# Optimization experiments

Measured on AMD Instinct MI355X. Metric: run time of the kernel, lower is better.

Reference implementation:

```python
import jax, jax.numpy as jnp
import numpy as np

B, T, E, H = 2, 2048, 768, 12
DH = E // H  # per-head attention dim
EPS = 1e-5


def setup_inputs() -> dict:
    key = jax.random.key(0)
    ks = jax.random.split(key, 12)
    s = 0.02
    return {
        "x": jax.random.normal(ks[0], (B, T, E), dtype=jnp.float32),
        # stacked per-head projection weights: [H, E, DH], biases [H, DH]
        "Wq": jax.random.normal(ks[1], (H, E, DH), dtype=jnp.float32) * s,
        "bq": jax.random.normal(ks[2], (H, DH), dtype=jnp.float32) * s,
        "Wk": jax.random.normal(ks[3], (H, E, DH), dtype=jnp.float32) * s,
        "bk": jax.random.normal(ks[4], (H, DH), dtype=jnp.float32) * s,
        "Wv": jax.random.normal(ks[5], (H, E, DH), dtype=jnp.float32) * s,
        "bv": jax.random.normal(ks[6], (H, DH), dtype=jnp.float32) * s,
        "Wo": jax.random.normal(ks[7], (E, E), dtype=jnp.float32) * s,
        "bo": jax.random.normal(ks[8], (E,), dtype=jnp.float32) * s,
        "gamma": jnp.ones((E,), dtype=jnp.float32),
        "beta": jnp.zeros((E,), dtype=jnp.float32),
    }


def reference(x, Wq, bq, Wk, bk, Wv, bv, Wo, bo, gamma, beta):
    # per-head projections (heads stacked on axis h)
    q = jnp.einsum("bte,hed->bhtd", x, Wq) + bq[None, :, None, :]
    k = jnp.einsum("bte,hed->bhtd", x, Wk) + bk[None, :, None, :]
    v = jnp.einsum("bte,hed->bhtd", x, Wv) + bv[None, :, None, :]

    scores = jnp.einsum("bhtd,bhsd->bhts", q, k) / jnp.sqrt(jnp.float32(DH))
    causal = jnp.tril(jnp.ones((T, T), dtype=bool))  # True = keep
    scores = jnp.where(causal[None, None], scores, -jnp.inf)
    attn = jax.nn.softmax(scores, axis=-1)
    o = jnp.einsum("bhts,bhsd->bhtd", attn, v)  # [B,H,T,DH]

    # concat heads in head order -> [B,T,E]
    concat = jnp.transpose(o, (0, 2, 1, 3)).reshape(B, T, E)
    proj = concat @ Wo + bo

    # LayerNorm(proj) then residual add
    mu = jnp.mean(proj, axis=-1, keepdims=True)
    var = jnp.mean((proj - mu) ** 2, axis=-1, keepdims=True)
    normed = (proj - mu) * jax.lax.rsqrt(var + EPS) * gamma + beta
    return x + normed
```

## Files before the change

### kernel.cpp

```cpp
#include <hip/hip_runtime.h>
#include <stdint.h>

#define NROWS 4096
#define EMB   768
#define NQKV  2304
#define TSEQ  2048
#define NHEAD 12
#define NBH   24

typedef unsigned short u16;
typedef u16  ushort8 __attribute__((ext_vector_type(8)));
typedef __bf16 bf16x8 __attribute__((ext_vector_type(8)));
typedef float f32x4 __attribute__((ext_vector_type(4)));

typedef const __attribute__((address_space(1))) void* gas_ptr;
typedef __attribute__((address_space(3))) void* las_ptr;

__device__ __forceinline__ u16 f2bf(float f) {
  union { float f; uint32_t u; } v; v.f = f;
  uint32_t u = v.u;
  return (u16)((u + 0x7fffu + ((u >> 16) & 1u)) >> 16);
}
__device__ __forceinline__ uint32_t cvtpk(float lo, float hi) {
  uint32_t r;
  asm("v_cvt_pk_bf16_f32 %0, %1, %2" : "=v"(r) : "v"(lo), "v"(hi));
  return r;
}

#define VMCNT2 asm volatile("s_waitcnt vmcnt(2)" ::: "memory")
#define VMCNT0 asm volatile("s_waitcnt vmcnt(0)" ::: "memory")
#define LGKM0  asm volatile("s_waitcnt lgkmcnt(0)" ::: "memory")
#define SBAR   __builtin_amdgcn_s_barrier()
#define SCHED0 __builtin_amdgcn_sched_barrier(0)

__global__ __launch_bounds__(256) void k_pack_x(const float* __restrict__ x, u16* __restrict__ xb) {
  int i = (blockIdx.x * 256 + threadIdx.x) * 8;
  float4 a = *(const float4*)(x + i);
  float4 b = *(const float4*)(x + i + 4);
  uint4 o;
  o.x = cvtpk(a.x, a.y); o.y = cvtpk(a.z, a.w);
  o.z = cvtpk(b.x, b.y); o.w = cvtpk(b.z, b.w);
  *(uint4*)(xb + i) = o;
}

__global__ __launch_bounds__(256) void k_pack_wqkv(const float* __restrict__ Wq, const float* __restrict__ Wk,
                            const float* __restrict__ Wv, const float* __restrict__ bq,
                            const float* __restrict__ bk, const float* __restrict__ bv,
                            u16* __restrict__ wt, float* __restrict__ bias) {
  int idx = blockIdx.x * 256 + threadIdx.x;
  if (idx >= NQKV * EMB) return;
  int n = idx / EMB, e = idx - n * EMB;
  int sel = n / EMB;
  int c = n - sel * EMB;
  int h = c >> 6, d = c & 63;
  const float* W = sel == 0 ? Wq : (sel == 1 ? Wk : Wv);
  wt[idx] = f2bf(W[((size_t)h * EMB + e) * 64 + d]);
  if (e == 0) {
    const float* bs = sel == 0 ? bq : (sel == 1 ? bk : bv);
    bias[n] = bs[h * 64 + d];
  }
}

__global__ __launch_bounds__(256) void k_pack_wo(const float* __restrict__ Wo, u16* __restrict__ wot) {
  int idx = blockIdx.x * 256 + threadIdx.x;
  if (idx >= EMB * EMB) return;
  int n = idx / EMB, e = idx - n * EMB;
  wot[idx] = f2bf(Wo[(size_t)e * EMB + n]);
}

template<int OUT_F32>
__global__ __launch_bounds__(256) void k_gemm(const u16* __restrict__ A, const u16* __restrict__ Bt,
                                              const float* __restrict__ bias, void* __restrict__ Cout,
                                              int M, int N, int K) {
  __shared__ u16 lds_a[128 * 32];
  __shared__ u16 lds_b[128 * 32];
  int tid = threadIdx.x;
  int w = tid >> 6, lane = tid & 63;
  int wr = w >> 1, wc = w & 1;
  int m0 = blockIdx.x * 128, n0 = blockIdx.y * 128;
  int lrow = lane & 15, lk8 = (lane >> 4) * 8;

  f32x4 zero = {0.f, 0.f, 0.f, 0.f};
  f32x4 acc[4][4];
  for (int m = 0; m < 4; ++m) for (int n = 0; n < 4; ++n) acc[m][n] = zero;

  int sr = tid >> 2;
  int sk = (tid & 3) * 8;

  for (int k0 = 0; k0 < K; k0 += 32) {
#pragma unroll
    for (int c = 0; c < 2; ++c) {
      int r = c * 64 + sr;
      const u16* ga = A  + (size_t)(m0 + r) * K + k0 + sk;
      const u16* gb = Bt + (size_t)(n0 + r) * K + k0 + sk;
      u16* la = lds_a + c * 2048 + w * 512;
      u16* lb = lds_b + c * 2048 + w * 512;
      __builtin_amdgcn_global_load_lds((gas_ptr)ga, (las_ptr)la, 16, 0, 0);
      __builtin_amdgcn_global_load_lds((gas_ptr)gb, (las_ptr)lb, 16, 0, 0);
    }
    __syncthreads();
    bf16x8 af[4], bfr[4];
#pragma unroll
    for (int m = 0; m < 4; ++m)
      af[m] = *(const bf16x8*)(lds_a + (wr * 64 + m * 16 + lrow) * 32 + lk8);
#pragma unroll
    for (int n = 0; n < 4; ++n)
      bfr[n] = *(const bf16x8*)(lds_b + (wc * 64 + n * 16 + lrow) * 32 + lk8);
#pragma unroll
    for (int m = 0; m < 4; ++m)
#pragma unroll
      for (int n = 0; n < 4; ++n)
        acc[m][n] = __builtin_amdgcn_mfma_f32_16x16x32_bf16(af[m], bfr[n], acc[m][n], 0, 0, 0);
    __syncthreads();
  }

#pragma unroll
  for (int m = 0; m < 4; ++m)
#pragma unroll
    for (int n = 0; n < 4; ++n) {
      int col = n0 + wc * 64 + n * 16 + lrow;
      float bcol = bias[col];
#pragma unroll
      for (int r = 0; r < 4; ++r) {
        int row = m0 + wr * 64 + m * 16 + (lane >> 4) * 4 + r;
        float v = acc[m][n][r] + bcol;
        if (OUT_F32) ((float*)Cout)[(size_t)row * N + col] = v;
        else         ((u16*)Cout)[(size_t)row * N + col] = f2bf(v);
      }
    }
}

__global__ __launch_bounds__(256) void k_transpose_v(const u16* __restrict__ qkv, u16* __restrict__ vt) {
  __shared__ u16 lds[64][65];
  int bh = blockIdx.y;
  int b = bh / NHEAD, h = bh - b * NHEAD;
  int t0 = blockIdx.x * 64;
  int tid = threadIdx.x;
  int r = tid >> 2, c0 = (tid & 3) * 16;
  const u16* src = qkv + (size_t)(b * TSEQ + t0 + r) * NQKV + 2 * EMB + h * 64 + c0;
  ushort8 v0 = *(const ushort8*)(src);
  ushort8 v1 = *(const ushort8*)(src + 8);
#pragma unroll
  for (int j = 0; j < 8; ++j) { lds[r][c0 + j] = v0[j]; lds[r][c0 + 8 + j] = v1[j]; }
  __syncthreads();
  int d = tid >> 2, tt = (tid & 3) * 16;
  ushort8 o0, o1;
#pragma unroll
  for (int j = 0; j < 8; ++j) { o0[j] = lds[tt + j][d]; o1[j] = lds[tt + 8 + j][d]; }
  u16* dst = vt + (size_t)(bh * 64 + d) * TSEQ + t0 + tt;
  *(ushort8*)dst = o0;
  *(ushort8*)(dst + 8) = o1;
}

__global__ __launch_bounds__(256) void k_attn(const u16* __restrict__ qkv, const u16* __restrict__ vt,
                                              u16* __restrict__ aout) {
  __shared__ u16 kbuf[3][64 * 64];
  __shared__ u16 vbuf[2][64 * 64];
  __shared__ u16 pbuf[4][16 * 64];
  int tid = threadIdx.x;
  int w = tid >> 6, lane = tid & 63;
  int ql = lane & 15, g = lane >> 4;
  int bid = blockIdx.x;
  int xcd = bid & 7, slot = bid >> 3;
  int y = xcd * 3 + (slot >> 5);
  int qblk = 31 - (slot & 31);
  int b = y / NHEAD, h = y - b * NHEAD;
  int nt = qblk + 1;
  int qrow0w = qblk * 64 + w * 16;
  int qg = qrow0w + ql;

  const u16* qp = qkv + (size_t)(b * TSEQ + qg) * NQKV + h * 64;
  bf16x8 bq0 = *(const bf16x8*)(qp + g * 8);
  bf16x8 bq1 = *(const bf16x8*)(qp + 32 + g * 8);

  const u16* kst = qkv + (size_t)(b * TSEQ) * NQKV + EMB + h * 64;
  const u16* vst = vt + (size_t)y * 64 * TSEQ;
  int srow = tid >> 3, scol = tid & 7;

  f32x4 zero = {0.f, 0.f, 0.f, 0.f};
  f32x4 o[4]; for (int n = 0; n < 4; ++n) o[n] = zero;
  float lr = 0.f;
  const float sc2 = 0.18033688f;
  u16* pw = &pbuf[w][0];
  int swz = (ql & 7) << 3;

  auto STAGE_K = [&](int bi, int t_) {
#pragma unroll
    for (int i = 0; i < 2; ++i) {
      int row = i * 32 + srow;
      int c16 = scol ^ (row & 7);
      const u16* gk = kst + (size_t)(t_ * 64 + row) * NQKV + c16 * 8;
      __builtin_amdgcn_global_load_lds((gas_ptr)gk, (las_ptr)(&kbuf[bi][i * 2048 + w * 512]), 16, 0, 0);
    }
  };
  auto STAGE_V = [&](int bi, int t_) {
#pragma unroll
    for (int i = 0; i < 2; ++i) {
      int row = i * 32 + srow;
      int c16 = scol ^ (row & 7);
      const u16* gv = vst + (size_t)row * TSEQ + t_ * 64 + c16 * 8;
      __builtin_amdgcn_global_load_lds((gas_ptr)gv, (las_ptr)(&vbuf[bi][i * 2048 + w * 512]), 16, 0, 0);
    }
  };

  STAGE_V(0, 0);
  STAGE_K(0, 0);
  if (nt > 1) STAGE_K(1, 1);

  for (int t = 0; t < nt; ++t) {
    if (t + 1 < nt) VMCNT2; else VMCNT0;
    SBAR;
    if (t + 1 < nt) STAGE_V((t + 1) & 1, t + 1);
    if (t + 2 < nt) STAGE_K((t + 2) % 3, t + 2);

    const u16* kb = &kbuf[t % 3][0];
    const u16* vb = &vbuf[t & 1][0];
    int s0 = t * 64;

    f32x4 st[4];
#pragma unroll
    for (int sblk = 0; sblk < 4; ++sblk) {
      int row = sblk * 16 + ql;
      bf16x8 ka0 = *(const bf16x8*)(kb + ((row * 64 + 8 * g) ^ swz));
      bf16x8 ka1 = *(const bf16x8*)(kb + ((row * 64 + 32 + 8 * g) ^ swz));
      f32x4 acc = zero;
      acc = __builtin_amdgcn_mfma_f32_16x16x32_bf16(ka0, bq0, acc, 0, 0, 0);
      acc = __builtin_amdgcn_mfma_f32_16x16x32_bf16(ka1, bq1, acc, 0, 0, 0);
      st[sblk] = acc;
    }

    bool lastt = (t == nt - 1);
    float e[4][4];
#pragma unroll
    for (int sblk = 0; sblk < 4; ++sblk)
#pragma unroll
      for (int r = 0; r < 4; ++r) {
        float vv = __builtin_fmaf(st[sblk][r], sc2, -2.0f);
        if (lastt) {
          int sg = s0 + sblk * 16 + 4 * g + r;
          if (sg > qg) vv = -1e30f;
        }
        float ee = __builtin_amdgcn_exp2f(vv);
        e[sblk][r] = ee;
        lr += ee;
      }

#pragma unroll
    for (int sblk = 0; sblk < 4; ++sblk) {
      uint2 dw;
      dw.x = cvtpk(e[sblk][0], e[sblk][1]);
      dw.y = cvtpk(e[sblk][2], e[sblk][3]);
      *(uint2*)(pw + ((ql * 64 + sblk * 16 + 4 * g) ^ swz)) = dw;
    }
    LGKM0; SCHED0;
    bf16x8 ap0 = *(const bf16x8*)(pw + ((ql * 64 + 8 * g) ^ swz));
    bf16x8 ap1 = *(const bf16x8*)(pw + ((ql * 64 + 32 + 8 * g) ^ swz));

#pragma unroll
    for (int n = 0; n < 4; ++n) {
      int row = n * 16 + ql;
      bf16x8 vb0 = *(const bf16x8*)(vb + ((row * 64 + 8 * g) ^ swz));
      bf16x8 vb1 = *(const bf16x8*)(vb + ((row * 64 + 32 + 8 * g) ^ swz));
      o[n] = __builtin_amdgcn_mfma_f32_16x16x32_bf16(ap0, vb0, o[n], 0, 0, 0);
      o[n] = __builtin_amdgcn_mfma_f32_16x16x32_bf16(ap1, vb1, o[n], 0, 0, 0);
    }
  }

  lr += __shfl_xor(lr, 16);
  lr += __shfl_xor(lr, 32);
  float linv = 1.0f / lr;
  float li[4];
#pragma unroll
  for (int r = 0; r < 4; ++r) li[r] = __shfl(linv, 4 * g + r);
#pragma unroll
  for (int n = 0; n < 4; ++n)
#pragma unroll
    for (int r = 0; r < 4; ++r) {
      int q = qrow0w + 4 * g + r;
      aout[(size_t)(b * TSEQ + q) * EMB + h * 64 + n * 16 + ql] = f2bf(o[n][r] * li[r]);
    }
}

__global__ __launch_bounds__(256) void k_ln_res(const float* __restrict__ proj, const float* __restrict__ x,
                                                const float* __restrict__ gamma, const float* __restrict__ beta,
                                                float* __restrict__ out) {
  __shared__ float smem[2][4];
  int row = blockIdx.x;
  const float* pr = proj + (size_t)row * EMB;
  const float* xr = x + (size_t)row * EMB;
  float* orow = out + (size_t)row * EMB;
  int tid = threadIdx.x;
  float v[3];
  float s = 0.f, s2 = 0.f;
#pragma unroll
  for (int i = 0; i < 3; ++i) { v[i] = pr[tid + 256 * i]; s += v[i]; s2 += v[i] * v[i]; }
#pragma unroll
  for (int m = 1; m < 64; m <<= 1) { s += __shfl_xor(s, m); s2 += __shfl_xor(s2, m); }
  int w = tid >> 6, lane = tid & 63;
  if (lane == 0) { smem[0][w] = s; smem[1][w] = s2; }
  __syncthreads();
  s  = smem[0][0] + smem[0][1] + smem[0][2] + smem[0][3];
  s2 = smem[1][0] + smem[1][1] + smem[1][2] + smem[1][3];
  float mu = s * (1.f / EMB);
  float var = s2 * (1.f / EMB) - mu * mu;
  float rstd = rsqrtf(var + 1e-5f);
#pragma unroll
  for (int i = 0; i < 3; ++i) {
    int c = tid + 256 * i;
    orow[c] = xr[c] + (v[i] - mu) * rstd * gamma[c] + beta[c];
  }
}

extern "C" void kernel_launch(void* const* d_in, const int* in_sizes, int n_in,
                              void* d_out, int out_size, void* d_ws, size_t ws_size,
                              hipStream_t stream) {
  const float* x     = (const float*)d_in[0];
  const float* Wq    = (const float*)d_in[1];
  const float* bq    = (const float*)d_in[2];
  const float* Wk    = (const float*)d_in[3];
  const float* bk    = (const float*)d_in[4];
  const float* Wv    = (const float*)d_in[5];
  const float* bv    = (const float*)d_in[6];
  const float* Wo    = (const float*)d_in[7];
  const float* bo    = (const float*)d_in[8];
  const float* gamma = (const float*)d_in[9];
  const float* beta  = (const float*)d_in[10];
  float* out = (float*)d_out;

  char* ws = (char*)d_ws;
  size_t off = 0;
  u16* xb    = (u16*)(ws + off); off += (size_t)NROWS * EMB * 2;
  u16* wqkvt = (u16*)(ws + off); off += (size_t)NQKV * EMB * 2;
  u16* wot   = (u16*)(ws + off); off += (size_t)EMB * EMB * 2;
  float* bqkv = (float*)(ws + off); off += (size_t)NQKV * 4;
  u16* qkv   = (u16*)(ws + off); off += (size_t)NROWS * NQKV * 2;
  u16* vt    = (u16*)(ws + off); off += (size_t)NBH * 64 * TSEQ * 2;
  u16* aout  = (u16*)(ws + off); off += (size_t)NROWS * EMB * 2;
  float* proj = (float*)qkv;

  k_pack_x<<<NROWS * EMB / (256 * 8), 256, 0, stream>>>(x, xb);
  k_pack_wqkv<<<(NQKV * EMB + 255) / 256, 256, 0, stream>>>(Wq, Wk, Wv, bq, bk, bv, wqkvt, bqkv);
  k_pack_wo<<<(EMB * EMB + 255) / 256, 256, 0, stream>>>(Wo, wot);
  k_gemm<0><<<dim3(NROWS / 128, NQKV / 128), 256, 0, stream>>>(xb, wqkvt, bqkv, qkv, NROWS, NQKV, EMB);
  k_transpose_v<<<dim3(TSEQ / 64, NBH), 256, 0, stream>>>(qkv, vt);
  k_attn<<<dim3(768), 256, 0, stream>>>(qkv, vt, aout);
  k_gemm<1><<<dim3(NROWS / 128, EMB / 128), 256, 0, stream>>>(aout, wot, bo, proj, NROWS, EMB, EMB);
  k_ln_res<<<NROWS, 256, 0, stream>>>(proj, x, gamma, beta, out);
}
```

Baseline: 137.8 us.

## Fuse V transpose into QKV GEMM, persistent attention scheduler, swizzled K=64 GEMM tiles

The QKV GEMM epilogue now writes V directly in transposed layout, which removes the separate transpose kernel. The GEMM moves to a K-step of 64 with XOR-swizzled LDS tiles and is templated on tile shape, so the output projection can use 128x64 tiles for more blocks. Attention becomes a persistent kernel that pulls work from per-XCD atomic counters, giving dynamic load balance across the causal triangle. Its K/V staging is simplified to a double buffer with a full vmcnt(0) wait, which may expose more load latency than the previous triple-buffered K.

```diff
diff --git a/kernel.cpp b/kernel.cpp
--- a/kernel.cpp
+++ b/kernel.cpp
@@ -9,6 +9,7 @@
 #define NBH   24
 
 typedef unsigned short u16;
+typedef u16  ushort4v __attribute__((ext_vector_type(4)));
 typedef u16  ushort8 __attribute__((ext_vector_type(8)));
 typedef __bf16 bf16x8 __attribute__((ext_vector_type(8)));
 typedef float f32x4 __attribute__((ext_vector_type(4)));
@@ -27,11 +28,14 @@
   return r;
 }
 
-#define VMCNT2 asm volatile("s_waitcnt vmcnt(2)" ::: "memory")
 #define VMCNT0 asm volatile("s_waitcnt vmcnt(0)" ::: "memory")
 #define LGKM0  asm volatile("s_waitcnt lgkmcnt(0)" ::: "memory")
 #define SBAR   __builtin_amdgcn_s_barrier()
 #define SCHED0 __builtin_amdgcn_sched_barrier(0)
+
+__global__ void k_zero(uint32_t* cnt) {
+  if (threadIdx.x < 8) cnt[threadIdx.x] = 0;
+}
 
 __global__ __launch_bounds__(256) void k_pack_x(const float* __restrict__ x, u16* __restrict__ xb) {
   int i = (blockIdx.x * 256 + threadIdx.x) * 8;
@@ -68,217 +72,225 @@
   wot[idx] = f2bf(Wo[(size_t)e * EMB + n]);
 }
 
-template<int OUT_F32>
+template<int BM, int BN, int OUT_MODE>
 __global__ __launch_bounds__(256) void k_gemm(const u16* __restrict__ A, const u16* __restrict__ Bt,
                                               const float* __restrict__ bias, void* __restrict__ Cout,
-                                              int M, int N, int K) {
-  __shared__ u16 lds_a[128 * 32];
-  __shared__ u16 lds_b[128 * 32];
+                                              u16* __restrict__ vtout, int M, int N, int K) {
+  constexpr int MR = BM / 32, NR = BN / 32;
+  __shared__ u16 lds_a[BM * 64];
+  __shared__ u16 lds_b[BN * 64];
   int tid = threadIdx.x;
   int w = tid >> 6, lane = tid & 63;
   int wr = w >> 1, wc = w & 1;
-  int m0 = blockIdx.x * 128, n0 = blockIdx.y * 128;
-  int lrow = lane & 15, lk8 = (lane >> 4) * 8;
+  int m0 = blockIdx.x * BM, n0 = blockIdx.y * BN;
+  int lrow = lane & 15, g = lane >> 4;
 
   f32x4 zero = {0.f, 0.f, 0.f, 0.f};
-  f32x4 acc[4][4];
-  for (int m = 0; m < 4; ++m) for (int n = 0; n < 4; ++n) acc[m][n] = zero;
-
-  int sr = tid >> 2;
-  int sk = (tid & 3) * 8;
-
-  for (int k0 = 0; k0 < K; k0 += 32) {
-#pragma unroll
-    for (int c = 0; c < 2; ++c) {
-      int r = c * 64 + sr;
-      const u16* ga = A  + (size_t)(m0 + r) * K + k0 + sk;
-      const u16* gb = Bt + (size_t)(n0 + r) * K + k0 + sk;
-      u16* la = lds_a + c * 2048 + w * 512;
-      u16* lb = lds_b + c * 2048 + w * 512;
-      __builtin_amdgcn_global_load_lds((gas_ptr)ga, (las_ptr)la, 16, 0, 0);
-      __builtin_amdgcn_global_load_lds((gas_ptr)gb, (las_ptr)lb, 16, 0, 0);
+  f32x4 acc[MR][NR];
+  for (int m = 0; m < MR; ++m) for (int n = 0; n < NR; ++n) acc[m][n] = zero;
+
+  int l8 = lane >> 3, c8 = lane & 7;
+
+  for (int k0 = 0; k0 < K; k0 += 64) {
+#pragma unroll
+    for (int i = 0; i < BM / 32; ++i) {
+      int row = w * (BM / 4) + 8 * i + l8;
+      int c16 = c8 ^ (row & 7);
+      const u16* ga = A + (size_t)(m0 + row) * K + k0 + c16 * 8;
+      __builtin_amdgcn_global_load_lds((gas_ptr)ga, (las_ptr)(lds_a + (w * (BM / 4) + 8 * i) * 64), 16, 0, 0);
+    }
+#pragma unroll
+    for (int i = 0; i < BN / 32; ++i) {
+      int row = w * (BN / 4) + 8 * i + l8;
+      int c16 = c8 ^ (row & 7);
+      const u16* gb = Bt + (size_t)(n0 + row) * K + k0 + c16 * 8;
+      __builtin_amdgcn_global_load_lds((gas_ptr)gb, (las_ptr)(lds_b + (w * (BN / 4) + 8 * i) * 64), 16, 0, 0);
     }
     __syncthreads();
-    bf16x8 af[4], bfr[4];
-#pragma unroll
-    for (int m = 0; m < 4; ++m)
-      af[m] = *(const bf16x8*)(lds_a + (wr * 64 + m * 16 + lrow) * 32 + lk8);
-#pragma unroll
-    for (int n = 0; n < 4; ++n)
-      bfr[n] = *(const bf16x8*)(lds_b + (wc * 64 + n * 16 + lrow) * 32 + lk8);
-#pragma unroll
-    for (int m = 0; m < 4; ++m)
-#pragma unroll
-      for (int n = 0; n < 4; ++n)
-        acc[m][n] = __builtin_amdgcn_mfma_f32_16x16x32_bf16(af[m], bfr[n], acc[m][n], 0, 0, 0);
+    bf16x8 af[MR][2], bfr[NR][2];
+#pragma unroll
+    for (int m = 0; m < MR; ++m)
+#pragma unroll
+      for (int kc = 0; kc < 2; ++kc) {
+        int row = wr * (BM / 2) + m * 16 + lrow;
+        int ch = (kc * 4 + g) ^ (row & 7);
+        af[m][kc] = *(const bf16x8*)(lds_a + row * 64 + ch * 8);
+      }
+#pragma unroll
+    for (int n = 0; n < NR; ++n)
+#pragma unroll
+      for (int kc = 0; kc < 2; ++kc) {
+        int row = wc * (BN / 2) + n * 16 + lrow;
+        int ch = (kc * 4 + g) ^ (row & 7);
+        bfr[n][kc] = *(const bf16x8*)(lds_b + row * 64 + ch * 8);
+      }
+#pragma unroll
+    for (int kc = 0; kc < 2; ++kc)
+#pragma unroll
+      for (int m = 0; m < MR; ++m)
+#pragma unroll
+        for (int n = 0; n < NR; ++n)
+          acc[m][n] = __builtin_amdgcn_mfma_f32_16x16x32_bf16(af[m][kc], bfr[n][kc], acc[m][n], 0, 0, 0);
     __syncthreads();
   }
 
 #pragma unroll
-  for (int m = 0; m < 4; ++m)
-#pragma unroll
-    for (int n = 0; n < 4; ++n) {
-      int col = n0 + wc * 64 + n * 16 + lrow;
+  for (int m = 0; m < MR; ++m)
+#pragma unroll
+    for (int n = 0; n < NR; ++n) {
+      int col = n0 + wc * (BN / 2) + n * 16 + lrow;
       float bcol = bias[col];
-#pragma unroll
-      for (int r = 0; r < 4; ++r) {
-        int row = m0 + wr * 64 + m * 16 + (lane >> 4) * 4 + r;
-        float v = acc[m][n][r] + bcol;
-        if (OUT_F32) ((float*)Cout)[(size_t)row * N + col] = v;
-        else         ((u16*)Cout)[(size_t)row * N + col] = f2bf(v);
+      int row0 = m0 + wr * (BM / 2) + m * 16 + 4 * g;
+      if (OUT_MODE == 2 && col >= 2 * EMB) {
+        int c = col - 2 * EMB;
+        int hh = c >> 6, d = c & 63;
+        int bb = row0 >> 11, t = row0 & 2047;
+        int y = bb * NHEAD + hh;
+        ushort4v pk;
+#pragma unroll
+        for (int r = 0; r < 4; ++r) pk[r] = f2bf(acc[m][n][r] + bcol);
+        *(ushort4v*)(vtout + (size_t)(y * 64 + d) * TSEQ + t) = pk;
+      } else {
+#pragma unroll
+        for (int r = 0; r < 4; ++r) {
+          int row = row0 + r;
+          float v = acc[m][n][r] + bcol;
+          if (OUT_MODE == 1) ((float*)Cout)[(size_t)row * N + col] = v;
+          else               ((u16*)Cout)[(size_t)row * N + col] = f2bf(v);
+        }
       }
     }
 }
 
-__global__ __launch_bounds__(256) void k_transpose_v(const u16* __restrict__ qkv, u16* __restrict__ vt) {
-  __shared__ u16 lds[64][65];
-  int bh = blockIdx.y;
-  int b = bh / NHEAD, h = bh - b * NHEAD;
-  int t0 = blockIdx.x * 64;
-  int tid = threadIdx.x;
-  int r = tid >> 2, c0 = (tid & 3) * 16;
-  const u16* src = qkv + (size_t)(b * TSEQ + t0 + r) * NQKV + 2 * EMB + h * 64 + c0;
-  ushort8 v0 = *(const ushort8*)(src);
-  ushort8 v1 = *(const ushort8*)(src + 8);
-#pragma unroll
-  for (int j = 0; j < 8; ++j) { lds[r][c0 + j] = v0[j]; lds[r][c0 + 8 + j] = v1[j]; }
-  __syncthreads();
-  int d = tid >> 2, tt = (tid & 3) * 16;
-  ushort8 o0, o1;
-#pragma unroll
-  for (int j = 0; j < 8; ++j) { o0[j] = lds[tt + j][d]; o1[j] = lds[tt + 8 + j][d]; }
-  u16* dst = vt + (size_t)(bh * 64 + d) * TSEQ + t0 + tt;
-  *(ushort8*)dst = o0;
-  *(ushort8*)(dst + 8) = o1;
-}
-
-__global__ __launch_bounds__(256) void k_attn(const u16* __restrict__ qkv, const u16* __restrict__ vt,
-                                              u16* __restrict__ aout) {
-  __shared__ u16 kbuf[3][64 * 64];
+__global__ __launch_bounds__(256, 4) void k_attn(const u16* __restrict__ qkv, const u16* __restrict__ vt,
+                                                 u16* __restrict__ aout, uint32_t* __restrict__ cnt) {
+  __shared__ u16 kbuf[2][64 * 64];
   __shared__ u16 vbuf[2][64 * 64];
   __shared__ u16 pbuf[4][16 * 64];
+  __shared__ int task_s;
   int tid = threadIdx.x;
   int w = tid >> 6, lane = tid & 63;
   int ql = lane & 15, g = lane >> 4;
-  int bid = blockIdx.x;
-  int xcd = bid & 7, slot = bid >> 3;
-  int y = xcd * 3 + (slot >> 5);
-  int qblk = 31 - (slot & 31);
-  int b = y / NHEAD, h = y - b * NHEAD;
-  int nt = qblk + 1;
-  int qrow0w = qblk * 64 + w * 16;
-  int qg = qrow0w + ql;
-
-  const u16* qp = qkv + (size_t)(b * TSEQ + qg) * NQKV + h * 64;
-  bf16x8 bq0 = *(const bf16x8*)(qp + g * 8);
-  bf16x8 bq1 = *(const bf16x8*)(qp + 32 + g * 8);
-
-  const u16* kst = qkv + (size_t)(b * TSEQ) * NQKV + EMB + h * 64;
-  const u16* vst = vt + (size_t)y * 64 * TSEQ;
-  int srow = tid >> 3, scol = tid & 7;
-
-  f32x4 zero = {0.f, 0.f, 0.f, 0.f};
-  f32x4 o[4]; for (int n = 0; n < 4; ++n) o[n] = zero;
-  float lr = 0.f;
+  int xcd = blockIdx.x & 7;
   const float sc2 = 0.18033688f;
   u16* pw = &pbuf[w][0];
   int swz = (ql & 7) << 3;
-
-  auto STAGE_K = [&](int bi, int t_) {
-#pragma unroll
-    for (int i = 0; i < 2; ++i) {
-      int row = i * 32 + srow;
-      int c16 = scol ^ (row & 7);
-      const u16* gk = kst + (size_t)(t_ * 64 + row) * NQKV + c16 * 8;
-      __builtin_amdgcn_global_load_lds((gas_ptr)gk, (las_ptr)(&kbuf[bi][i * 2048 + w * 512]), 16, 0, 0);
+  int l8 = lane >> 3, c8 = lane & 7;
+
+  for (;;) {
+    if (tid == 0) task_s = (int)atomicAdd(&cnt[xcd], 1u);
+    __syncthreads();
+    int tau = task_s;
+    __syncthreads();
+    if (tau >= 96) break;
+
+    int idx = tau / 3;
+    int yl = tau - idx * 3;
+    int qb = 31 - idx;
+    int y = xcd * 3 + yl;
+    int b = y / NHEAD, h = y - b * NHEAD;
+    int nt = qb + 1;
+    int qrow0w = qb * 64 + w * 16;
+    int qg = qrow0w + ql;
+
+    const u16* qp = qkv + (size_t)(b * TSEQ + qg) * NQKV + h * 64;
+    bf16x8 bq0 = *(const bf16x8*)(qp + g * 8);
+    bf16x8 bq1 = *(const bf16x8*)(qp + 32 + g * 8);
+
+    const u16* kst = qkv + (size_t)(b * TSEQ) * NQKV + EMB + h * 64;
+    const u16* vst = vt + (size_t)y * 64 * TSEQ;
+
+    f32x4 zero = {0.f, 0.f, 0.f, 0.f};
+    f32x4 o[4]; for (int n = 0; n < 4; ++n) o[n] = zero;
+    float lr = 0.f;
+
+    auto STAGE = [&](int bi, int t_) {
+#pragma unroll
+      for (int i = 0; i < 2; ++i) {
+        int row = i * 32 + 8 * w + l8;
+        int c16 = c8 ^ (row & 7);
+        const u16* gk = kst + (size_t)(t_ * 64 + row) * NQKV + c16 * 8;
+        __builtin_amdgcn_global_load_lds((gas_ptr)gk, (las_ptr)(&kbuf[bi][(i * 32 + 8 * w) * 64]), 16, 0, 0);
+        const u16* gv = vst + (size_t)row * TSEQ + t_ * 64 + c16 * 8;
+        __builtin_amdgcn_global_load_lds((gas_ptr)gv, (las_ptr)(&vbuf[bi][(i * 32 + 8 * w) * 64]), 16, 0, 0);
+      }
+    };
+
+    STAGE(0, 0);
+    for (int t = 0; t < nt; ++t) {
+      int cur = t & 1;
+      VMCNT0;
+      SBAR;
+      if (t + 1 < nt) STAGE(cur ^ 1, t + 1);
+
+      const u16* kb = &kbuf[cur][0];
+      const u16* vb = &vbuf[cur][0];
+      int s0 = t * 64;
+
+      f32x4 st[4];
+#pragma unroll
+      for (int sblk = 0; sblk < 4; ++sblk) {
+        int row = sblk * 16 + ql;
+        bf16x8 ka0 = *(const bf16x8*)(kb + ((row * 64 + 8 * g) ^ swz));
+        bf16x8 ka1 = *(const bf16x8*)(kb + ((row * 64 + 32 + 8 * g) ^ swz));
+        f32x4 acc = zero;
+        acc = __builtin_amdgcn_mfma_f32_16x16x32_bf16(ka0, bq0, acc, 0, 0, 0);
+        acc = __builtin_amdgcn_mfma_f32_16x16x32_bf16(ka1, bq1, acc, 0, 0, 0);
+        st[sblk] = acc;
+      }
+
+      bool lastt = (t == nt - 1);
+      float e[4][4];
+#pragma unroll
+      for (int sblk = 0; sblk < 4; ++sblk)
+#pragma unroll
+        for (int r = 0; r < 4; ++r) {
+          float vv = __builtin_fmaf(st[sblk][r], sc2, -2.0f);
+          if (lastt) {
+            int sg = s0 + sblk * 16 + 4 * g + r;
+            if (sg > qg) vv = -1e30f;
+          }
+          float ee = __builtin_amdgcn_exp2f(vv);
+          e[sblk][r] = ee;
+          lr += ee;
+        }
+
+#pragma unroll
+      for (int sblk = 0; sblk < 4; ++sblk) {
+        uint2 dw;
+        dw.x = cvtpk(e[sblk][0], e[sblk][1]);
+        dw.y = cvtpk(e[sblk][2], e[sblk][3]);
+        *(uint2*)(pw + ((ql * 64 + sblk * 16 + 4 * g) ^ swz)) = dw;
+      }
+      LGKM0; SCHED0;
+      bf16x8 ap0 = *(const bf16x8*)(pw + ((ql * 64 + 8 * g) ^ swz));
+      bf16x8 ap1 = *(const bf16x8*)(pw + ((ql * 64 + 32 + 8 * g) ^ swz));
+
+#pragma unroll
+      for (int n = 0; n < 4; ++n) {
+        int row = n * 16 + ql;
+        bf16x8 vb0 = *(const bf16x8*)(vb + ((row * 64 + 8 * g) ^ swz));
+        bf16x8 vb1 = *(const bf16x8*)(vb + ((row * 64 + 32 + 8 * g) ^ swz));
+        o[n] = __builtin_amdgcn_mfma_f32_16x16x32_bf16(ap0, vb0, o[n], 0, 0, 0);
+        o[n] = __builtin_amdgcn_mfma_f32_16x16x32_bf16(ap1, vb1, o[n], 0, 0, 0);
+      }
     }
-  };
-  auto STAGE_V = [&](int bi, int t_) {
-#pragma unroll
-    for (int i = 0; i < 2; ++i) {
-      int row = i * 32 + srow;
-      int c16 = scol ^ (row & 7);
-      const u16* gv = vst + (size_t)row * TSEQ + t_ * 64 + c16 * 8;
-      __builtin_amdgcn_global_load_lds((gas_ptr)gv, (las_ptr)(&vbuf[bi][i * 2048 + w * 512]), 16, 0, 0);
-    }
-  };
-
-  STAGE_V(0, 0);
-  STAGE_K(0, 0);
-  if (nt > 1) STAGE_K(1, 1);
-
-  for (int t = 0; t < nt; ++t) {
-    if (t + 1 < nt) VMCNT2; else VMCNT0;
-    SBAR;
-    if (t + 1 < nt) STAGE_V((t + 1) & 1, t + 1);
-    if (t + 2 < nt) STAGE_K((t + 2) % 3, t + 2);
-
-    const u16* kb = &kbuf[t % 3][0];
-    const u16* vb = &vbuf[t & 1][0];
-    int s0 = t * 64;
-
-    f32x4 st[4];
-#pragma unroll
-    for (int sblk = 0; sblk < 4; ++sblk) {
-      int row = sblk * 16 + ql;
-      bf16x8 ka0 = *(const bf16x8*)(kb + ((row * 64 + 8 * g) ^ swz));
-      bf16x8 ka1 = *(const bf16x8*)(kb + ((row * 64 + 32 + 8 * g) ^ swz));
-      f32x4 acc = zero;
-      acc = __builtin_amdgcn_mfma_f32_16x16x32_bf16(ka0, bq0, acc, 0, 0, 0);
-      acc = __builtin_amdgcn_mfma_f32_16x16x32_bf16(ka1, bq1, acc, 0, 0, 0);
-      st[sblk] = acc;
-    }
-
-    bool lastt = (t == nt - 1);
-    float e[4][4];
-#pragma unroll
-    for (int sblk = 0; sblk < 4; ++sblk)
+
+    float lw = lr;
+    lw += __shfl_xor(lw, 16);
+    lw += __shfl_xor(lw, 32);
+    float linv = 1.0f / lw;
+    float li[4];
+#pragma unroll
+    for (int r = 0; r < 4; ++r) li[r] = __shfl(linv, 4 * g + r);
+#pragma unroll
+    for (int n = 0; n < 4; ++n)
 #pragma unroll
       for (int r = 0; r < 4; ++r) {
-        float vv = __builtin_fmaf(st[sblk][r], sc2, -2.0f);
-        if (lastt) {
-          int sg = s0 + sblk * 16 + 4 * g + r;
-          if (sg > qg) vv = -1e30f;
-        }
-        float ee = __builtin_amdgcn_exp2f(vv);
-        e[sblk][r] = ee;
-        lr += ee;
-      }
-
-#pragma unroll
-    for (int sblk = 0; sblk < 4; ++sblk) {
-      uint2 dw;
-      dw.x = cvtpk(e[sblk][0], e[sblk][1]);
-      dw.y = cvtpk(e[sblk][2], e[sblk][3]);
-      *(uint2*)(pw + ((ql * 64 + sblk * 16 + 4 * g) ^ swz)) = dw;
-    }
-    LGKM0; SCHED0;
-    bf16x8 ap0 = *(const bf16x8*)(pw + ((ql * 64 + 8 * g) ^ swz));
-    bf16x8 ap1 = *(const bf16x8*)(pw + ((ql * 64 + 32 + 8 * g) ^ swz));
-
-#pragma unroll
-    for (int n = 0; n < 4; ++n) {
-      int row = n * 16 + ql;
-      bf16x8 vb0 = *(const bf16x8*)(vb + ((row * 64 + 8 * g) ^ swz));
-      bf16x8 vb1 = *(const bf16x8*)(vb + ((row * 64 + 32 + 8 * g) ^ swz));
-      o[n] = __builtin_amdgcn_mfma_f32_16x16x32_bf16(ap0, vb0, o[n], 0, 0, 0);
-      o[n] = __builtin_amdgcn_mfma_f32_16x16x32_bf16(ap1, vb1, o[n], 0, 0, 0);
-    }
+        int q = qrow0w + 4 * g + r;
+        aout[(size_t)(b * TSEQ + q) * EMB + h * 64 + n * 16 + ql] = f2bf(o[n][r] * li[r]);
+      }
   }
-
-  lr += __shfl_xor(lr, 16);
-  lr += __shfl_xor(lr, 32);
-  float linv = 1.0f / lr;
-  float li[4];
-#pragma unroll
-  for (int r = 0; r < 4; ++r) li[r] = __shfl(linv, 4 * g + r);
-#pragma unroll
-  for (int n = 0; n < 4; ++n)
-#pragma unroll
-    for (int r = 0; r < 4; ++r) {
-      int q = qrow0w + 4 * g + r;
-      aout[(size_t)(b * TSEQ + q) * EMB + h * 64 + n * 16 + ql] = f2bf(o[n][r] * li[r]);
-    }
 }
 
 __global__ __launch_bounds__(256) void k_ln_res(const float* __restrict__ proj, const float* __restrict__ x,
@@ -333,17 +345,18 @@
   u16* wqkvt = (u16*)(ws + off); off += (size_t)NQKV * EMB * 2;
   u16* wot   = (u16*)(ws + off); off += (size_t)EMB * EMB * 2;
   float* bqkv = (float*)(ws + off); off += (size_t)NQKV * 4;
+  uint32_t* cnt = (uint32_t*)(ws + off); off += 64;
   u16* qkv   = (u16*)(ws + off); off += (size_t)NROWS * NQKV * 2;
   u16* vt    = (u16*)(ws + off); off += (size_t)NBH * 64 * TSEQ * 2;
   u16* aout  = (u16*)(ws + off); off += (size_t)NROWS * EMB * 2;
   float* proj = (float*)qkv;
 
+  k_zero<<<1, 64, 0, stream>>>(cnt);
   k_pack_x<<<NROWS * EMB / (256 * 8), 256, 0, stream>>>(x, xb);
   k_pack_wqkv<<<(NQKV * EMB + 255) / 256, 256, 0, stream>>>(Wq, Wk, Wv, bq, bk, bv, wqkvt, bqkv);
   k_pack_wo<<<(EMB * EMB + 255) / 256, 256, 0, stream>>>(Wo, wot);
-  k_gemm<0><<<dim3(NROWS / 128, NQKV / 128), 256, 0, stream>>>(xb, wqkvt, bqkv, qkv, NROWS, NQKV, EMB);
-  k_transpose_v<<<dim3(TSEQ / 64, NBH), 256, 0, stream>>>(qkv, vt);
-  k_attn<<<dim3(768), 256, 0, stream>>>(qkv, vt, aout);
-  k_gemm<1><<<dim3(NROWS / 128, EMB / 128), 256, 0, stream>>>(aout, wot, bo, proj, NROWS, EMB, EMB);
+  k_gemm<128, 128, 2><<<dim3(NROWS / 128, NQKV / 128), 256, 0, stream>>>(xb, wqkvt, bqkv, qkv, vt, NROWS, NQKV, EMB);
+  k_attn<<<dim3(1024), 256, 0, stream>>>(qkv, vt, aout, cnt);
+  k_gemm<128, 64, 1><<<dim3(NROWS / 128, EMB / 64), 256, 0, stream>>>(aout, wot, bo, proj, nullptr, NROWS, EMB, EMB);
   k_ln_res<<<NROWS, 256, 0, stream>>>(proj, x, gamma, beta, out);
 }
```

Result: faster. 134.9 us (-2.1%).
